# Kernel optimization log

Measured on AMD Instinct MI355X. Metric: run time of the kernel, lower is better.

Reference implementation:

```python
import jax, jax.numpy as jnp
import numpy as np

C_ATOM = 128; C_PAIR = 16; H = 4; DH = 32; BQ = 32; BK = 128
N_ATOMS = 11776; NB = N_ATOMS // BQ; N_TOK = 512
C_TOK = 384; C_TP = 128; C_TP_IN = 32; N_LAYERS = 3

def _ln(x):
    mu = jnp.mean(x, axis=-1, keepdims=True)
    xc = x - mu
    var = jnp.mean(xc * xc, axis=-1, keepdims=True)
    return xc * jax.lax.rsqrt(var + 1e-5)

def setup_inputs():
    key = jax.random.key(0)
    ks = jax.random.split(key, 32)
    rn = lambda k, s, sc=0.02: jax.random.normal(k, s, jnp.float32) * sc
    q_idx = jnp.arange(N_ATOMS, dtype=jnp.int32).reshape(NB, BQ)
    centers = jnp.arange(NB, dtype=jnp.int32) * BQ + BQ // 2
    win = centers[:, None] + jnp.arange(-BK // 2, BK // 2, dtype=jnp.int32)[None, :]
    k_mask = (win >= 0) & (win < N_ATOMS)
    k_idx = jnp.clip(win, 0, N_ATOMS - 1)
    return {
        'atom_feats': jax.random.normal(ks[0], (1, N_ATOMS, C_ATOM), jnp.float32),
        'token_pair_feats': jax.random.normal(ks[1], (1, N_TOK, N_TOK, C_TP_IN), jnp.float32),
        'W_cond': rn(ks[2], (C_ATOM, C_ATOM)),
        'W_ph': rn(ks[3], (C_PAIR, C_ATOM)),
        'W_pw': rn(ks[4], (C_PAIR, C_ATOM)),
        'W_mlp1': rn(ks[5], (C_PAIR, C_PAIR)),
        'W_mlp2': rn(ks[6], (C_PAIR, C_PAIR)),
        'pb_ln_w': jnp.ones((C_PAIR,), jnp.float32),
        'pb_ln_b': jnp.zeros((C_PAIR,), jnp.float32),
        'pb_w': rn(ks[7], (H, C_PAIR)),
        'sln_w': rn(ks[8], (N_LAYERS, 2 * C_ATOM, C_ATOM)),
        'qkv_w': rn(ks[9], (N_LAYERS, 3 * C_ATOM, C_ATOM)),
        'q_bias': rn(ks[10], (N_LAYERS, C_ATOM)),
        'out_w': rn(ks[11], (N_LAYERS, C_ATOM, C_ATOM)),
        'out_b': jnp.zeros((N_LAYERS, C_ATOM), jnp.float32),
        'ada_w': rn(ks[12], (N_LAYERS, 2 * C_ATOM, C_ATOM)),
        'ta_w': rn(ks[13], (N_LAYERS, 4 * C_ATOM, C_ATOM)),
        'tb_w': rn(ks[14], (N_LAYERS, C_ATOM, 2 * C_ATOM)),
        'gate_w': rn(ks[15], (N_LAYERS, C_ATOM, C_ATOM)),
        'gate_b': jnp.full((N_LAYERS, C_ATOM), -2.0, jnp.float32),
        'W_tok': rn(ks[16], (C_TOK, C_ATOM)),
        'W_trunk': rn(ks[17], (C_TOK, C_TOK)),
        'W_struct': rn(ks[18], (C_TOK, C_TOK)),
        'W_pairin': rn(ks[19], (C_TP, C_TP_IN)),
        'W_outer': rn(ks[20], (2 * C_TP, C_TOK)),
        'q_idx': q_idx, 'k_idx': k_idx, 'k_mask': k_mask,
        'atom_to_token': jnp.sort(jax.random.randint(ks[21], (N_ATOMS,), 0, N_TOK, dtype=jnp.int32)),
    }

def _forward(atom_feats, token_pair_feats, W_cond, W_ph, W_pw, W_mlp1, W_mlp2,
             pb_ln_w, pb_ln_b, pb_w, sln_w, qkv_w, q_bias, out_w, out_b,
             ada_w, ta_w, tb_w, gate_w, gate_b, W_tok, W_trunk, W_struct,
             W_pairin, W_outer, q_idx, k_idx, k_mask, atom_to_token):
    c = atom_feats @ W_cond.T                       # [1,N,128] atom conditioning
    s_ln = _ln(c)                                   # shared normed conditioning
    # ---- blocked pair representation + pair-to-bias ----
    cq = jax.nn.relu(s_ln[:, q_idx])                # [1,NB,BQ,128]
    ck = jax.nn.relu(s_ln[:, k_idx])                # [1,NB,BK,128]
    p = (cq @ W_ph.T)[:, :, :, None, :] + (ck @ W_pw.T)[:, :, None, :, :]  # [1,NB,BQ,BK,16]
    p = p + jax.nn.relu(jax.nn.relu(p) @ W_mlp1.T) @ W_mlp2.T
    pb = (_ln(p) * pb_ln_w + pb_ln_b) @ pb_w.T      # [1,NB,BQ,BK,H]
    pb = jnp.transpose(pb, (0, 1, 4, 2, 3))         # [1,NB,H,BQ,BK]
    neg = jnp.where(k_mask[None, :, None, None, :], 0.0, -1e9)
    a = c
    scale = 1.0 / np.sqrt(DH).astype(np.float32)
    for l in range(N_LAYERS):
        # blocked local attention with AdaLN-conditioned input
        gb = s_ln @ sln_w[l].T
        x = jax.nn.sigmoid(gb[..., :C_ATOM]) * _ln(a) + gb[..., C_ATOM:]
        qkv = x @ qkv_w[l].T
        q, k, v = jnp.split(qkv, 3, axis=-1)
        q = (q + q_bias[l]).reshape(1, N_ATOMS, H, DH)
        k = k.reshape(1, N_ATOMS, H, DH)
        v = v.reshape(1, N_ATOMS, H, DH)
        qb = q[:, q_idx]; kb = k[:, k_idx]; vb = v[:, k_idx]
        sc = jnp.einsum('bnqhd,bnkhd->bnhqk', qb, kb) * scale + pb + neg
        att = jax.nn.softmax(sc, axis=-1)
        o = jnp.einsum('bnhqk,bnkhd->bnqhd', att, vb).reshape(1, N_ATOMS, C_ATOM)
        a = a + o @ out_w[l].T + out_b[l]
        # AdaLN-modulated SwiGLU transition with adaLN-zero gate (bias init -2)
        gb2 = s_ln @ ada_w[l].T
        xt = jax.nn.sigmoid(gb2[..., :C_ATOM]) * _ln(a) + gb2[..., C_ATOM:]
        ab = xt @ ta_w[l].T
        g = jax.nn.silu(ab[..., :2 * C_ATOM]) * ab[..., 2 * C_ATOM:]
        h = g @ tb_w[l].T
        gate = jax.nn.sigmoid(s_ln @ gate_w[l].T + gate_b[l])
        a = a + gate * h
    # ---- atom -> token aggregation and output projections ----
    atom_out = jax.nn.relu(a @ W_tok.T)             # [1,N,384]
    sums = jax.ops.segment_sum(atom_out[0], atom_to_token, num_segments=N_TOK)
    cnt = jax.ops.segment_sum(jnp.ones((N_ATOMS,), atom_out.dtype), atom_to_token, num_segments=N_TOK)
    tok = (sums / jnp.maximum(cnt, 1.0)[:, None])[None]  # [1,T,384]
    s_trunk = tok @ W_trunk.T
    s_struct = tok @ W_struct.T
    u = tok @ W_outer.T                              # [1,T,256]
    pair = token_pair_feats @ W_pairin.T + u[..., :C_TP][:, :, None, :] + u[..., C_TP:][:, None, :, :]
    return s_trunk, s_struct, pair

def reference(atom_feats, token_pair_feats, W_cond, W_ph, W_pw, W_mlp1, W_mlp2,
              pb_ln_w, pb_ln_b, pb_w, sln_w, qkv_w, q_bias, out_w, out_b,
              ada_w, ta_w, tb_w, gate_w, gate_b, W_tok, W_trunk, W_struct,
              W_pairin, W_outer, q_idx, k_idx, k_mask, atom_to_token):
    return _forward(atom_feats, token_pair_feats, W_cond, W_ph, W_pw, W_mlp1, W_mlp2,
                    pb_ln_w, pb_ln_b, pb_w, sln_w, qkv_w, q_bias, out_w, out_b,
                    ada_w, ta_w, tb_w, gate_w, gate_b, W_tok, W_trunk, W_struct,
                    W_pairin, W_outer, q_idx, k_idx, k_mask, atom_to_token)
```

## Files before the change

kernel.cpp:

```cpp
#include <hip/hip_runtime.h>
#include <cstddef>

typedef unsigned short u16;
typedef __attribute__((ext_vector_type(8))) short bf8;
typedef __attribute__((ext_vector_type(4))) float f4;
typedef __attribute__((ext_vector_type(4))) unsigned short us4;

#define NATOMS 11776
#define NBLK   368

__device__ __forceinline__ u16 f2b(float x){
  union { float f; unsigned u; } v; v.f = x;
  unsigned r = v.u + 0x7fffu + ((v.u >> 16) & 1u);
  return (u16)(r >> 16);
}
__device__ __forceinline__ float b2f(u16 x){
  union { unsigned u; float f; } v; v.u = ((unsigned)x) << 16;
  return v.f;
}
__device__ __forceinline__ f4 f4zero(){ f4 z = {0.f,0.f,0.f,0.f}; return z; }
__device__ __forceinline__ f4 mfma16(bf8 a, bf8 b, f4 c){
  return __builtin_amdgcn_mfma_f32_16x16x32_bf16(a, b, c, 0, 0, 0);
}
__device__ __forceinline__ int iclamp(int v, int lo, int hi){ return v < lo ? lo : (v > hi ? hi : v); }
__device__ __forceinline__ void lds_fence(){
  asm volatile("s_waitcnt lgkmcnt(0)" ::: "memory");
  __builtin_amdgcn_sched_barrier(0);
}

struct CvtArgs {
  const float* src[13];
  u16* dst[13];
  int n4[13];
};

__global__ __launch_bounds__(256) void k_convert(CvtArgs a){
  int stride = gridDim.x * 256;
  int tid = blockIdx.x * 256 + threadIdx.x;
  for (int s = 0; s < 13; ++s){
    const float4* src = (const float4*)a.src[s];
    us4* dst = (us4*)a.dst[s];
    int n = a.n4[s];
    for (int i = tid; i < n; i += stride){
      float4 v = src[i];
      us4 o;
      o.x = f2b(v.x); o.y = f2b(v.y); o.z = f2b(v.z); o.w = f2b(v.w);
      dst[i] = o;
    }
  }
}

template<int N, int K, int LDA = K>
__device__ __forceinline__ void gemm_strip(const u16* __restrict__ A, const u16* __restrict__ W, float* L){
  constexpr int CPW = N / 4;
  constexpr int T = CPW / 16;
  const int lane = threadIdx.x & 63;
  const int wave = threadIdx.x >> 6;
  const int rr = lane & 15, grp = lane >> 4;
  f4 acc[T];
#pragma unroll
  for (int t = 0; t < T; ++t) acc[t] = f4zero();
#pragma unroll
  for (int kc = 0; kc < K / 32; ++kc){
    bf8 af = *(const bf8*)(A + rr * LDA + kc * 32 + grp * 8);
#pragma unroll
    for (int t = 0; t < T; ++t){
      const u16* wp = W + (size_t)(wave * CPW + t * 16 + rr) * K + kc * 32 + grp * 8;
      acc[t] = mfma16(af, *(const bf8*)wp, acc[t]);
    }
  }
#pragma unroll
  for (int t = 0; t < T; ++t)
#pragma unroll
    for (int r = 0; r < 4; ++r)
      L[(grp * 4 + r) * N + wave * CPW + t * 16 + rr] = acc[t][r];
}

template<int N, int K>
__global__ __launch_bounds__(256) void k_gemm_f32(const u16* __restrict__ A, const u16* __restrict__ W,
                                                  float* __restrict__ out){
  __shared__ float L[16 * N];
  const int strip = blockIdx.x;
  gemm_strip<N, K>(A + (size_t)strip * 16 * K, W, L);
  __syncthreads();
  const size_t base = (size_t)strip * 16 * N;
  for (int i = threadIdx.x; i < 16 * N; i += 256) out[base + i] = L[i];
}

__global__ __launch_bounds__(256) void k_pre(const u16* __restrict__ sln, const float* __restrict__ lnA,
                                             const u16* __restrict__ slnW, const u16* __restrict__ gateW,
                                             const u16* __restrict__ qkvW, const float* __restrict__ qb,
                                             const float* __restrict__ gbias,
                                             u16* __restrict__ qkv_out, float* __restrict__ gate_out){
  __shared__ float LB[16 * 384];
  __shared__ __align__(16) u16 X[16 * 136];
  const int strip = blockIdx.x;
  const u16* Ag = sln + (size_t)strip * 2048;
  gemm_strip<256, 128>(Ag, slnW, LB);
  __syncthreads();
  for (int i = threadIdx.x; i < 2048; i += 256){
    int r = i >> 7, c = i & 127;
    float g1 = LB[r * 256 + c], g2 = LB[r * 256 + 128 + c];
    float s = 1.f / (1.f + __expf(-g1));
    X[r * 136 + c] = f2b(s * lnA[(size_t)(strip * 16 + r) * 128 + c] + g2);
  }
  __syncthreads();
  gemm_strip<128, 128>(Ag, gateW, LB);
  __syncthreads();
  for (int i = threadIdx.x; i < 2048; i += 256){
    int c = i & 127;
    gate_out[(size_t)strip * 2048 + i] = 1.f / (1.f + __expf(-(LB[i] + gbias[c])));
  }
  __syncthreads();
  gemm_strip<384, 128, 136>(X, qkvW, LB);
  __syncthreads();
  const float scale = 0.17677669529663687f;
  for (int i = threadIdx.x; i < 16 * 384; i += 256){
    int r = i / 384, c = i - r * 384;
    float v = LB[i];
    if (c < 128) v = (v + qb[c]) * scale;
    qkv_out[(size_t)(strip * 16 + r) * 384 + c] = f2b(v);
  }
}

template<int LAST>
__global__ __launch_bounds__(256) void k_post(const u16* __restrict__ sln, float* __restrict__ lnA,
                                              float* __restrict__ a, const float* __restrict__ gate,
                                              const u16* __restrict__ adaW, const u16* __restrict__ taW,
                                              const u16* __restrict__ tbW, const u16* __restrict__ tokW,
                                              float* __restrict__ atom_out){
  __shared__ float LB[16 * 512];
  __shared__ __align__(16) u16 X[16 * 136];
  __shared__ __align__(16) u16 G[16 * 264];
  const int strip = blockIdx.x;
  const u16* Ag = sln + (size_t)strip * 2048;
  gemm_strip<256, 128>(Ag, adaW, LB);
  __syncthreads();
  for (int i = threadIdx.x; i < 2048; i += 256){
    int r = i >> 7, c = i & 127;
    float g1 = LB[r * 256 + c], g2 = LB[r * 256 + 128 + c];
    float s = 1.f / (1.f + __expf(-g1));
    X[r * 136 + c] = f2b(s * lnA[(size_t)(strip * 16 + r) * 128 + c] + g2);
  }
  __syncthreads();
  gemm_strip<512, 128, 136>(X, taW, LB);
  __syncthreads();
  for (int i = threadIdx.x; i < 16 * 256; i += 256){
    int r = i >> 8, c = i & 255;
    float ab1 = LB[r * 512 + c], ab2 = LB[r * 512 + 256 + c];
    G[r * 264 + c] = f2b(ab1 / (1.f + __expf(-ab1)) * ab2);
  }
  __syncthreads();
  gemm_strip<128, 256, 264>(G, tbW, LB);
  __syncthreads();
  for (int i = threadIdx.x; i < 2048; i += 256){
    size_t idx = (size_t)strip * 2048 + i;
    float v = a[idx] + gate[idx] * LB[i];
    a[idx] = v;
    LB[i] = v;
    if (LAST){ int r = i >> 7, c = i & 127; X[r * 136 + c] = f2b(v); }
  }
  __syncthreads();
  if (!LAST){
    int r = threadIdx.x >> 4, s = threadIdx.x & 15;
    float sum = 0.f, sq = 0.f;
#pragma unroll
    for (int j = 0; j < 8; ++j){ float v = LB[r * 128 + s * 8 + j]; sum += v; sq += v * v; }
#pragma unroll
    for (int m = 1; m < 16; m <<= 1){ sum += __shfl_xor(sum, m); sq += __shfl_xor(sq, m); }
    float mu = sum * (1.f / 128.f);
    float var = sq * (1.f / 128.f) - mu * mu;
    float rs = rsqrtf(var + 1e-5f);
#pragma unroll
    for (int j = 0; j < 8; ++j){
      int c = s * 8 + j;
      lnA[(size_t)(strip * 16 + r) * 128 + c] = (LB[r * 128 + c] - mu) * rs;
    }
  } else {
    gemm_strip<384, 128, 136>(X, tokW, LB);
    __syncthreads();
    const size_t base = (size_t)strip * 16 * 384;
    for (int i = threadIdx.x; i < 16 * 384; i += 256) atom_out[base + i] = fmaxf(LB[i], 0.f);
  }
}

__global__ __launch_bounds__(256) void k_ln_phpw(const float* __restrict__ c, float* __restrict__ lnA,
                                                 u16* __restrict__ slnb, const float* __restrict__ Wph,
                                                 const float* __restrict__ Wpw, float* __restrict__ ph,
                                                 float* __restrict__ pw){
  __shared__ float rs[4][128];
  const int wave = threadIdx.x >> 6, lane = threadIdx.x & 63;
  const int row = blockIdx.x * 4 + wave;
  const float* cr = c + (size_t)row * 128;
  float2 v = *(const float2*)(cr + lane * 2);
  float sum = v.x + v.y, sq = v.x * v.x + v.y * v.y;
#pragma unroll
  for (int m = 1; m < 64; m <<= 1){ sum += __shfl_xor(sum, m); sq += __shfl_xor(sq, m); }
  float mu = sum * (1.f / 128.f);
  float var = sq * (1.f / 128.f) - mu * mu;
  float r = rsqrtf(var + 1e-5f);
  float s0 = (v.x - mu) * r, s1 = (v.y - mu) * r;
  size_t base = (size_t)row * 128 + lane * 2;
  lnA[base] = s0; lnA[base + 1] = s1;
  slnb[base] = f2b(s0); slnb[base + 1] = f2b(s1);
  rs[wave][lane * 2] = fmaxf(s0, 0.f); rs[wave][lane * 2 + 1] = fmaxf(s1, 0.f);
  __syncthreads();
  int h = lane & 15, part = lane >> 4;
  float acch = 0.f, accw = 0.f;
#pragma unroll
  for (int k = 0; k < 32; ++k){
    int kk = part * 32 + k;
    float rv = rs[wave][kk];
    acch += rv * Wph[h * 128 + kk];
    accw += rv * Wpw[h * 128 + kk];
  }
  acch += __shfl_xor(acch, 16); acch += __shfl_xor(acch, 32);
  accw += __shfl_xor(accw, 16); accw += __shfl_xor(accw, 32);
  if (lane < 16){
    ph[(size_t)row * 16 + h] = acch;
    pw[(size_t)row * 16 + h] = accw;
  }
}

__global__ __launch_bounds__(256) void k_pb(const float* __restrict__ ph, const float* __restrict__ pw,
                                            const float* __restrict__ W1, const float* __restrict__ W2,
                                            const float* __restrict__ lnw, const float* __restrict__ lnb,
                                            const float* __restrict__ pbw, float* __restrict__ bias){
  __shared__ __align__(16) u16 mt[4][16 * 24];
  __shared__ __align__(16) u16 vt[4][16 * 24];
  const int t = threadIdx.x;
  const int lane = t & 63, wave = t >> 6;
  const int rr = lane & 15, grp = lane >> 4;
  const int b = blockIdx.x >> 3, qg = blockIdx.x & 7;
  const int q = qg * 4 + wave;
  const int qa = b * 32 + q;

  bf8 wf1 = {0,0,0,0,0,0,0,0}, wf2 = {0,0,0,0,0,0,0,0};
  bf8 bproj = {0,0,0,0,0,0,0,0}, bones = {0,0,0,0,0,0,0,0};
  if (grp < 2){
#pragma unroll
    for (int j = 0; j < 8; ++j){
      wf1[j] = (short)f2b(W1[rr * 16 + grp * 8 + j]);
      wf2[j] = (short)f2b(W2[rr * 16 + grp * 8 + j]);
      bones[j] = (short)0x3F80;
    }
    if (rr < 4){
#pragma unroll
      for (int j = 0; j < 8; ++j)
        bproj[j] = (short)f2b(pbw[rr * 16 + grp * 8 + j] * lnw[grp * 8 + j]);
    }
  }
  float w2s_r = 0.f, bb_r = 0.f;
  if (rr < 4){
#pragma unroll
    for (int cc = 0; cc < 16; ++cc){
      float pv = pbw[rr * 16 + cc];
      w2s_r += pv * lnw[cc];
      bb_r  += pv * lnb[cc];
    }
  }
  const float* phq = ph + (size_t)qa * 16;
  float pha[8];
  if (grp < 2){
#pragma unroll
    for (int j = 0; j < 8; ++j) pha[j] = phq[grp * 8 + j];
  }
  const float ph_r = phq[rr];
  u16* mw = &mt[wave][0];
  u16* vw = &vt[wave][0];

  for (int kt = 0; kt < 8; ++kt){
    const int k0 = kt * 16;
    bf8 af = {0,0,0,0,0,0,0,0};
    if (grp < 2){
      int winA = b * 32 + k0 + rr - 48;
      int kaA = iclamp(winA, 0, NATOMS - 1);
      const float* pwr = pw + (size_t)kaA * 16 + grp * 8;
#pragma unroll
      for (int j = 0; j < 8; ++j) af[j] = (short)f2b(fmaxf(pha[j] + pwr[j], 0.f));
    }
    f4 c1 = mfma16(af, wf1, f4zero());
#pragma unroll
    for (int r = 0; r < 4; ++r)
      mw[(grp * 4 + r) * 24 + rr] = f2b(fmaxf(c1[r], 0.f));
    lds_fence();
    bf8 mf = {0,0,0,0,0,0,0,0};
    if (grp < 2) mf = *(const bf8*)(mw + rr * 24 + grp * 8);
    f4 c2 = mfma16(mf, wf2, f4zero());
#pragma unroll
    for (int r = 0; r < 4; ++r){
      int win = b * 32 + k0 + grp * 4 + r - 48;
      int ka = iclamp(win, 0, NATOMS - 1);
      float v = c2[r] + ph_r + pw[(size_t)ka * 16 + rr];
      vw[(grp * 4 + r) * 24 + rr] = f2b(v);
    }
    lds_fence();
    bf8 vf = {0,0,0,0,0,0,0,0}, vf2 = {0,0,0,0,0,0,0,0};
    if (grp < 2){
      vf = *(const bf8*)(vw + rr * 24 + grp * 8);
#pragma unroll
      for (int j = 0; j < 8; ++j){
        float x = b2f((u16)vf[j]);
        union { float f; unsigned u; } s; s.f = x * x;
        vf2[j] = (short)(u16)(s.u >> 16);
      }
    }
    f4 T1 = mfma16(vf, bproj, f4zero());
    f4 T2 = mfma16(vf, bones, f4zero());
    f4 T3 = mfma16(vf2, bones, f4zero());
    if (rr < 4){
      float4 o;
      float ov[4];
#pragma unroll
      for (int r = 0; r < 4; ++r){
        int win = b * 32 + k0 + grp * 4 + r - 48;
        bool valid = (win >= 0) && (win < NATOMS);
        float S = T2[r], Q = T3[r], d = T1[r];
        float mu = S * (1.f / 16.f);
        float var = Q * (1.f / 16.f) - mu * mu;
        float rq = rsqrtf(var + 1e-5f);
        ov[r] = rq * (d - mu * w2s_r) + bb_r + (valid ? 0.f : -1e9f);
      }
      o.x = ov[0]; o.y = ov[1]; o.z = ov[2]; o.w = ov[3];
      *(float4*)(bias + ((size_t)((b * 4 + rr) * 32) + q) * 128 + k0 + grp * 4) = o;
    }
  }
}

__global__ __launch_bounds__(256) void k_attn(const u16* __restrict__ qkv, const float* __restrict__ bias,
                                              const u16* __restrict__ outw, const float* __restrict__ outb,
                                              float* __restrict__ a, float* __restrict__ lnA){
  __shared__ u16 VT[128][136];
  __shared__ u16 P[4][32 * 136];
  __shared__ u16 O[32][136];
  __shared__ float aL[32][128];
  const int t = threadIdx.x;
  const int lane = t & 63, wave = t >> 6;
  const int b = blockIdx.x;
  const int rr = lane & 15, grp = lane >> 4;

  for (int i = 0; i < 8; ++i){
    int s = t + 256 * i;
    int ka = s & 127, d0 = (s >> 7) * 8;
    int win = b * 32 + ka - 48;
    int src = iclamp(win, 0, NATOMS - 1);
    bf8 v = *(const bf8*)(qkv + (size_t)src * 384 + 256 + d0);
#pragma unroll
    for (int j = 0; j < 8; ++j) VT[d0 + j][ka] = (u16)v[j];
  }
  __syncthreads();

  const int h = wave;
  bf8 kfr[8];
#pragma unroll
  for (int kt = 0; kt < 8; ++kt){
    int ka = kt * 16 + rr;
    int win = b * 32 + ka - 48;
    int src = iclamp(win, 0, NATOMS - 1);
    kfr[kt] = *(const bf8*)(qkv + (size_t)src * 384 + 128 + h * 32 + grp * 8);
  }
  f4 S[2][8];
#pragma unroll
  for (int qt = 0; qt < 2; ++qt){
    bf8 qf = *(const bf8*)(qkv + (size_t)(b * 32 + qt * 16 + rr) * 384 + h * 32 + grp * 8);
#pragma unroll
    for (int kt = 0; kt < 8; ++kt){
      S[qt][kt] = f4zero();
      S[qt][kt] = mfma16(qf, kfr[kt], S[qt][kt]);
    }
  }
  const float* brow = bias + (size_t)((b * 4 + h) * 32) * 128;
#pragma unroll
  for (int qt = 0; qt < 2; ++qt){
#pragma unroll
    for (int r = 0; r < 4; ++r){
      int q = qt * 16 + grp * 4 + r;
      float vals[8];
      float mx = -1e30f;
#pragma unroll
      for (int kt = 0; kt < 8; ++kt){
        float v = S[qt][kt][r] + brow[q * 128 + kt * 16 + rr];
        vals[kt] = v;
        mx = fmaxf(mx, v);
      }
#pragma unroll
      for (int m = 1; m < 16; m <<= 1) mx = fmaxf(mx, __shfl_xor(mx, m));
      float sum = 0.f;
#pragma unroll
      for (int kt = 0; kt < 8; ++kt){ vals[kt] = __expf(vals[kt] - mx); sum += vals[kt]; }
#pragma unroll
      for (int m = 1; m < 16; m <<= 1) sum += __shfl_xor(sum, m);
      float inv = 1.f / sum;
#pragma unroll
      for (int kt = 0; kt < 8; ++kt)
        P[h][q * 136 + kt * 16 + rr] = f2b(vals[kt] * inv);
    }
  }
  __syncthreads();
  f4 oacc[2][2];
#pragma unroll
  for (int qt = 0; qt < 2; ++qt)
#pragma unroll
    for (int dt = 0; dt < 2; ++dt) oacc[qt][dt] = f4zero();
#pragma unroll
  for (int kc = 0; kc < 4; ++kc){
#pragma unroll
    for (int qt = 0; qt < 2; ++qt){
      bf8 pa = *(const bf8*)(&P[h][(qt * 16 + rr) * 136 + kc * 32 + grp * 8]);
#pragma unroll
      for (int dt = 0; dt < 2; ++dt){
        bf8 vb = *(const bf8*)(&VT[h * 32 + dt * 16 + rr][kc * 32 + grp * 8]);
        oacc[qt][dt] = mfma16(pa, vb, oacc[qt][dt]);
      }
    }
  }
#pragma unroll
  for (int qt = 0; qt < 2; ++qt)
#pragma unroll
    for (int dt = 0; dt < 2; ++dt)
#pragma unroll
      for (int r = 0; r < 4; ++r)
        O[qt * 16 + grp * 4 + r][h * 32 + dt * 16 + rr] = f2b(oacc[qt][dt][r]);
  __syncthreads();
  f4 pacc[2][2];
#pragma unroll
  for (int qt = 0; qt < 2; ++qt)
#pragma unroll
    for (int ct = 0; ct < 2; ++ct) pacc[qt][ct] = f4zero();
#pragma unroll
  for (int kc = 0; kc < 4; ++kc){
    bf8 a0 = *(const bf8*)(&O[rr][kc * 32 + grp * 8]);
    bf8 a1 = *(const bf8*)(&O[16 + rr][kc * 32 + grp * 8]);
#pragma unroll
    for (int ct = 0; ct < 2; ++ct){
      bf8 wf = *(const bf8*)(outw + (size_t)(wave * 32 + ct * 16 + rr) * 128 + kc * 32 + grp * 8);
      pacc[0][ct] = mfma16(a0, wf, pacc[0][ct]);
      pacc[1][ct] = mfma16(a1, wf, pacc[1][ct]);
    }
  }
#pragma unroll
  for (int qt = 0; qt < 2; ++qt)
#pragma unroll
    for (int ct = 0; ct < 2; ++ct)
#pragma unroll
      for (int r = 0; r < 4; ++r){
        int q = qt * 16 + grp * 4 + r;
        int col = wave * 32 + ct * 16 + rr;
        size_t idx = (size_t)(b * 32 + q) * 128 + col;
        float v = a[idx] + pacc[qt][ct][r] + outb[col];
        a[idx] = v;
        aL[q][col] = v;
      }
  __syncthreads();
  {
    int r = t >> 3, s8 = t & 7;
    float sum = 0.f, sq = 0.f;
#pragma unroll
    for (int j = 0; j < 16; ++j){ float v = aL[r][s8 * 16 + j]; sum += v; sq += v * v; }
#pragma unroll
    for (int m = 1; m < 8; m <<= 1){ sum += __shfl_xor(sum, m); sq += __shfl_xor(sq, m); }
    float mu = sum * (1.f / 128.f);
    float var = sq * (1.f / 128.f) - mu * mu;
    float rs = rsqrtf(var + 1e-5f);
#pragma unroll
    for (int j = 0; j < 16; ++j){
      int c = s8 * 16 + j;
      lnA[(size_t)(b * 32 + r) * 128 + c] = (aL[r][c] - mu) * rs;
    }
  }
}

__device__ __forceinline__ int lbound(const int* __restrict__ arr, int n, int v){
  int lo = 0, hi = n;
  while (lo < hi){ int mid = (lo + hi) >> 1; if (arr[mid] < v) lo = mid + 1; else hi = mid; }
  return lo;
}

__global__ __launch_bounds__(256) void k_segmean(const float* __restrict__ atom_out,
                                                 const int* __restrict__ a2t, u16* __restrict__ tokbf){
  const int tok = blockIdx.x;
  __shared__ int lo_s, hi_s;
  if (threadIdx.x == 0){
    lo_s = lbound(a2t, NATOMS, tok);
    hi_s = lbound(a2t, NATOMS, tok + 1);
  }
  __syncthreads();
  int lo = lo_s, hi = hi_s;
  float inv = 1.f / fmaxf((float)(hi - lo), 1.f);
  for (int c = threadIdx.x; c < 384; c += 256){
    float s = 0.f;
    for (int aa = lo; aa < hi; ++aa) s += atom_out[(size_t)aa * 384 + c];
    tokbf[(size_t)tok * 384 + c] = f2b(s * inv);
  }
}

__global__ __launch_bounds__(256) void k_tok(const u16* __restrict__ tok, const u16* __restrict__ catW,
                                             float* __restrict__ s_trunk, float* __restrict__ s_struct,
                                             float* __restrict__ u_f){
  __shared__ float LB[16 * 1024];
  const int strip = blockIdx.x;
  gemm_strip<1024, 384>(tok + (size_t)strip * 16 * 384, catW, LB);
  __syncthreads();
  for (int i = threadIdx.x; i < 16 * 1024; i += 256){
    int r = i >> 10, c = i & 1023;
    int row = strip * 16 + r;
    float v = LB[i];
    if (c < 384) s_trunk[(size_t)row * 384 + c] = v;
    else if (c < 768) s_struct[(size_t)row * 384 + (c - 384)] = v;
    else u_f[(size_t)row * 256 + (c - 768)] = v;
  }
}

__global__ __launch_bounds__(256) void k_pair(const float* __restrict__ tpf, const float* __restrict__ Wp,
                                              const float* __restrict__ u, float* __restrict__ out){
  const int lane = threadIdx.x & 63, wave = threadIdx.x >> 6;
  const int rr = lane & 15, grp = lane >> 4;
  const int pairbase = blockIdx.x * 64 + wave * 16;
  const int i = (blockIdx.x * 64) >> 9;
  bf8 af;
  {
    const float* tr = tpf + (size_t)(pairbase + rr) * 32 + grp * 8;
#pragma unroll
    for (int j = 0; j < 8; ++j) af[j] = (short)f2b(tr[j]);
  }
  f4 acc[8];
#pragma unroll
  for (int t = 0; t < 8; ++t){
    bf8 bf;
    const float* wr = Wp + (size_t)(t * 16 + rr) * 32 + grp * 8;
#pragma unroll
    for (int j = 0; j < 8; ++j) bf[j] = (short)f2b(wr[j]);
    acc[t] = mfma16(af, bf, f4zero());
  }
  const float* ui = u + (size_t)i * 256;
#pragma unroll
  for (int t = 0; t < 8; ++t){
    int c = t * 16 + rr;
    float uic = ui[c];
#pragma unroll
    for (int r = 0; r < 4; ++r){
      int p = pairbase + grp * 4 + r;
      int j = p & 511;
      out[(size_t)p * 128 + c] = acc[t][r] + uic + u[(size_t)j * 256 + 128 + c];
    }
  }
}

extern "C" void kernel_launch(void* const* d_in, const int* in_sizes, int n_in,
                              void* d_out, int out_size, void* d_ws, size_t ws_size,
                              hipStream_t stream){
  (void)in_sizes; (void)n_in; (void)out_size; (void)ws_size;
  const float* atom_feats = (const float*)d_in[0];
  const float* tpf        = (const float*)d_in[1];
  const float* W_cond     = (const float*)d_in[2];
  const float* W_ph       = (const float*)d_in[3];
  const float* W_pw       = (const float*)d_in[4];
  const float* W_mlp1     = (const float*)d_in[5];
  const float* W_mlp2     = (const float*)d_in[6];
  const float* pb_ln_w    = (const float*)d_in[7];
  const float* pb_ln_b    = (const float*)d_in[8];
  const float* pb_w       = (const float*)d_in[9];
  const float* sln_w      = (const float*)d_in[10];
  const float* qkv_w      = (const float*)d_in[11];
  const float* q_bias     = (const float*)d_in[12];
  const float* out_w      = (const float*)d_in[13];
  const float* out_b      = (const float*)d_in[14];
  const float* ada_w      = (const float*)d_in[15];
  const float* ta_w       = (const float*)d_in[16];
  const float* tb_w       = (const float*)d_in[17];
  const float* gate_w     = (const float*)d_in[18];
  const float* gate_b     = (const float*)d_in[19];
  const float* W_tok      = (const float*)d_in[20];
  const float* W_trunk    = (const float*)d_in[21];
  const float* W_struct   = (const float*)d_in[22];
  const float* W_pairin   = (const float*)d_in[23];
  const float* W_outer    = (const float*)d_in[24];
  const int*   a2t        = (const int*)d_in[28];

  char* wsb = (char*)d_ws;
  size_t off = 0;
  auto alc = [&](size_t bytes) -> void* {
    void* r = wsb + off;
    off = (off + bytes + 255) & ~(size_t)255;
    return r;
  };

  u16* af_bf     = (u16*)alc((size_t)NATOMS * 128 * 2);
  u16* wcond_bf  = (u16*)alc(16384 * 2);
  u16* sln_bfw   = (u16*)alc(98304 * 2);
  u16* qkv_bfw   = (u16*)alc(147456 * 2);
  u16* out_bfw   = (u16*)alc(49152 * 2);
  u16* ada_bfw   = (u16*)alc(98304 * 2);
  u16* ta_bfw    = (u16*)alc(196608 * 2);
  u16* tb_bfw    = (u16*)alc(98304 * 2);
  u16* gate_bfw  = (u16*)alc(49152 * 2);
  u16* tok_bfw   = (u16*)alc(49152 * 2);
  u16* trunk_bfw = (u16*)alc(147456 * 2);
  u16* struct_bfw= (u16*)alc(147456 * 2);
  u16* outer_bfw = (u16*)alc(98304 * 2);
  float* a_f     = (float*)alc((size_t)NATOMS * 128 * 4);
  float* lnA     = (float*)alc((size_t)NATOMS * 128 * 4);
  u16* sln_bf    = (u16*)alc((size_t)NATOMS * 128 * 2);
  u16* qkv_bf    = (u16*)alc((size_t)NATOMS * 384 * 2);
  float* gate_f  = (float*)alc((size_t)NATOMS * 128 * 4);
  float* ph      = (float*)alc((size_t)NATOMS * 16 * 4);
  float* pw      = (float*)alc((size_t)NATOMS * 16 * 4);
  float* bias    = (float*)alc((size_t)NBLK * 4 * 32 * 128 * 4);
  float* atom_out= bias;
  u16* tok_bf    = (u16*)alc(512 * 384 * 2);
  float* u_f     = (float*)alc(512 * 256 * 4);

  float* s_trunk  = (float*)d_out;
  float* s_struct = s_trunk + 512 * 384;
  float* pair_out = s_struct + 512 * 384;

  CvtArgs ca;
  const float* srcs[13] = {atom_feats, W_cond, sln_w, qkv_w, out_w, ada_w, ta_w, tb_w,
                           gate_w, W_tok, W_trunk, W_struct, W_outer};
  u16* dsts[13] = {af_bf, wcond_bf, sln_bfw, qkv_bfw, out_bfw, ada_bfw, ta_bfw, tb_bfw,
                   gate_bfw, tok_bfw, trunk_bfw, struct_bfw, outer_bfw};
  int n4s[13] = {NATOMS * 128 / 4, 4096, 24576, 36864, 12288, 24576, 49152, 24576,
                 12288, 12288, 36864, 36864, 24576};
  for (int s = 0; s < 13; ++s){ ca.src[s] = srcs[s]; ca.dst[s] = dsts[s]; ca.n4[s] = n4s[s]; }
  k_convert<<<512, 256, 0, stream>>>(ca);

  k_gemm_f32<128, 128><<<736, 256, 0, stream>>>(af_bf, wcond_bf, a_f);
  k_ln_phpw<<<2944, 256, 0, stream>>>(a_f, lnA, sln_bf, W_ph, W_pw, ph, pw);
  k_pb<<<NBLK * 8, 256, 0, stream>>>(ph, pw, W_mlp1, W_mlp2, pb_ln_w, pb_ln_b, pb_w, bias);

  for (int l = 0; l < 3; ++l){
    const u16* slnW  = sln_bfw  + (size_t)l * 256 * 128;
    const u16* qkvW  = qkv_bfw  + (size_t)l * 384 * 128;
    const u16* outW  = out_bfw  + (size_t)l * 128 * 128;
    const u16* adaW  = ada_bfw  + (size_t)l * 256 * 128;
    const u16* taW   = ta_bfw   + (size_t)l * 512 * 128;
    const u16* tbW   = tb_bfw   + (size_t)l * 128 * 256;
    const u16* gateW = gate_bfw + (size_t)l * 128 * 128;
    k_pre<<<736, 256, 0, stream>>>(sln_bf, lnA, slnW, gateW, qkvW,
                                   q_bias + l * 128, gate_b + l * 128, qkv_bf, gate_f);
    k_attn<<<NBLK, 256, 0, stream>>>(qkv_bf, bias, outW, out_b + l * 128, a_f, lnA);
    if (l < 2)
      k_post<0><<<736, 256, 0, stream>>>(sln_bf, lnA, a_f, gate_f, adaW, taW, tbW,
                                         tok_bfw, atom_out);
    else
      k_post<1><<<736, 256, 0, stream>>>(sln_bf, lnA, a_f, gate_f, adaW, taW, tbW,
                                         tok_bfw, atom_out);
  }

  k_segmean<<<512, 256, 0, stream>>>(atom_out, a2t, tok_bf);
  k_tok<<<32, 256, 0, stream>>>(tok_bf, trunk_bfw, s_trunk, s_struct, u_f);
  k_pair<<<4096, 256, 0, stream>>>(tpf, W_pairin, u_f, pair_out);
}
```

Before: 433.9 us.

## Fuse cond GEMM with layernorm/pair projections, move gate into post, register LN in attn

Replaces the bf16 conversion of atom_feats, the separate W_cond GEMM and the LN/ph/pw kernel with one k_cond kernel that converts fp32 to bf16 on the fly and does LN plus the ph/pw projections via MFMA. The gate GEMM moves from k_pre into k_post and its values stay in registers, so the fp32 gate buffer is never written or read back. The attention epilogue computes the layernorm from registers with shuffles and a small partial-sum array instead of staging a 32x128 fp32 tile in LDS. This cuts launches and global traffic, at the cost of more register pressure in k_post and ph/pw now computed in bf16 instead of fp32.

```diff
diff --git a/kernel.cpp b/kernel.cpp
--- a/kernel.cpp
+++ b/kernel.cpp
@@ -27,17 +27,24 @@
   asm volatile("s_waitcnt lgkmcnt(0)" ::: "memory");
   __builtin_amdgcn_sched_barrier(0);
 }
+__device__ __forceinline__ bf8 cvt_f32x8(const float* __restrict__ p){
+  float4 a = *(const float4*)p, b = *(const float4*)(p + 4);
+  bf8 o;
+  o[0] = (short)f2b(a.x); o[1] = (short)f2b(a.y); o[2] = (short)f2b(a.z); o[3] = (short)f2b(a.w);
+  o[4] = (short)f2b(b.x); o[5] = (short)f2b(b.y); o[6] = (short)f2b(b.z); o[7] = (short)f2b(b.w);
+  return o;
+}
 
 struct CvtArgs {
-  const float* src[13];
-  u16* dst[13];
-  int n4[13];
+  const float* src[11];
+  u16* dst[11];
+  int n4[11];
 };
 
 __global__ __launch_bounds__(256) void k_convert(CvtArgs a){
   int stride = gridDim.x * 256;
   int tid = blockIdx.x * 256 + threadIdx.x;
-  for (int s = 0; s < 13; ++s){
+  for (int s = 0; s < 11; ++s){
     const float4* src = (const float4*)a.src[s];
     us4* dst = (us4*)a.dst[s];
     int n = a.n4[s];
@@ -76,22 +83,77 @@
       L[(grp * 4 + r) * N + wave * CPW + t * 16 + rr] = acc[t][r];
 }
 
-template<int N, int K>
-__global__ __launch_bounds__(256) void k_gemm_f32(const u16* __restrict__ A, const u16* __restrict__ W,
-                                                  float* __restrict__ out){
-  __shared__ float L[16 * N];
+__global__ __launch_bounds__(256) void k_cond(const float* __restrict__ af, const float* __restrict__ Wc,
+                                              const float* __restrict__ Wph, const float* __restrict__ Wpw,
+                                              float* __restrict__ a_f, float* __restrict__ lnA,
+                                              u16* __restrict__ sln_bf, float* __restrict__ ph,
+                                              float* __restrict__ pw){
+  __shared__ float LB[16 * 128];
+  __shared__ __align__(16) u16 X[16 * 136];
   const int strip = blockIdx.x;
-  gemm_strip<N, K>(A + (size_t)strip * 16 * K, W, L);
-  __syncthreads();
-  const size_t base = (size_t)strip * 16 * N;
-  for (int i = threadIdx.x; i < 16 * N; i += 256) out[base + i] = L[i];
+  const int lane = threadIdx.x & 63, wave = threadIdx.x >> 6;
+  const int rr = lane & 15, grp = lane >> 4;
+  {
+    f4 acc[2];
+    acc[0] = f4zero(); acc[1] = f4zero();
+#pragma unroll
+    for (int kc = 0; kc < 4; ++kc){
+      bf8 afr = cvt_f32x8(af + (size_t)(strip * 16 + rr) * 128 + kc * 32 + grp * 8);
+#pragma unroll
+      for (int t = 0; t < 2; ++t){
+        bf8 bfr = cvt_f32x8(Wc + (size_t)(wave * 32 + t * 16 + rr) * 128 + kc * 32 + grp * 8);
+        acc[t] = mfma16(afr, bfr, acc[t]);
+      }
+    }
+#pragma unroll
+    for (int t = 0; t < 2; ++t)
+#pragma unroll
+      for (int r = 0; r < 4; ++r)
+        LB[(grp * 4 + r) * 128 + wave * 32 + t * 16 + rr] = acc[t][r];
+  }
+  __syncthreads();
+  {
+    int r = threadIdx.x >> 4, s = threadIdx.x & 15;
+    float sum = 0.f, sq = 0.f;
+#pragma unroll
+    for (int j = 0; j < 8; ++j){ float v = LB[r * 128 + s * 8 + j]; sum += v; sq += v * v; }
+#pragma unroll
+    for (int m = 1; m < 16; m <<= 1){ sum += __shfl_xor(sum, m); sq += __shfl_xor(sq, m); }
+    float mu = sum * (1.f / 128.f);
+    float var = sq * (1.f / 128.f) - mu * mu;
+    float rs = rsqrtf(var + 1e-5f);
+#pragma unroll
+    for (int j = 0; j < 8; ++j){
+      int c = s * 8 + j;
+      float v = LB[r * 128 + c];
+      size_t idx = (size_t)(strip * 16 + r) * 128 + c;
+      a_f[idx] = v;
+      float ln = (v - mu) * rs;
+      lnA[idx] = ln;
+      sln_bf[idx] = f2b(ln);
+      X[r * 136 + c] = f2b(fmaxf(ln, 0.f));
+    }
+  }
+  __syncthreads();
+  if (wave < 2){
+    const float* Wsel = wave ? Wpw : Wph;
+    f4 acc = f4zero();
+#pragma unroll
+    for (int kc = 0; kc < 4; ++kc){
+      bf8 afr = *(const bf8*)(&X[rr * 136 + kc * 32 + grp * 8]);
+      bf8 bfr = cvt_f32x8(Wsel + (size_t)rr * 128 + kc * 32 + grp * 8);
+      acc = mfma16(afr, bfr, acc);
+    }
+    float* out = wave ? pw : ph;
+#pragma unroll
+    for (int r = 0; r < 4; ++r)
+      out[(size_t)(strip * 16 + grp * 4 + r) * 16 + rr] = acc[r];
+  }
 }
 
 __global__ __launch_bounds__(256) void k_pre(const u16* __restrict__ sln, const float* __restrict__ lnA,
-                                             const u16* __restrict__ slnW, const u16* __restrict__ gateW,
-                                             const u16* __restrict__ qkvW, const float* __restrict__ qb,
-                                             const float* __restrict__ gbias,
-                                             u16* __restrict__ qkv_out, float* __restrict__ gate_out){
+                                             const u16* __restrict__ slnW, const u16* __restrict__ qkvW,
+                                             const float* __restrict__ qb, u16* __restrict__ qkv_out){
   __shared__ float LB[16 * 384];
   __shared__ __align__(16) u16 X[16 * 136];
   const int strip = blockIdx.x;
@@ -103,13 +165,6 @@
     float g1 = LB[r * 256 + c], g2 = LB[r * 256 + 128 + c];
     float s = 1.f / (1.f + __expf(-g1));
     X[r * 136 + c] = f2b(s * lnA[(size_t)(strip * 16 + r) * 128 + c] + g2);
-  }
-  __syncthreads();
-  gemm_strip<128, 128>(Ag, gateW, LB);
-  __syncthreads();
-  for (int i = threadIdx.x; i < 2048; i += 256){
-    int c = i & 127;
-    gate_out[(size_t)strip * 2048 + i] = 1.f / (1.f + __expf(-(LB[i] + gbias[c])));
   }
   __syncthreads();
   gemm_strip<384, 128, 136>(X, qkvW, LB);
@@ -125,7 +180,8 @@
 
 template<int LAST>
 __global__ __launch_bounds__(256) void k_post(const u16* __restrict__ sln, float* __restrict__ lnA,
-                                              float* __restrict__ a, const float* __restrict__ gate,
+                                              float* __restrict__ a,
+                                              const u16* __restrict__ gateW, const float* __restrict__ gbias,
                                               const u16* __restrict__ adaW, const u16* __restrict__ taW,
                                               const u16* __restrict__ tbW, const u16* __restrict__ tokW,
                                               float* __restrict__ atom_out){
@@ -134,6 +190,16 @@
   __shared__ __align__(16) u16 G[16 * 264];
   const int strip = blockIdx.x;
   const u16* Ag = sln + (size_t)strip * 2048;
+  float gv[8];
+  gemm_strip<128, 128>(Ag, gateW, LB);
+  __syncthreads();
+#pragma unroll
+  for (int ii = 0; ii < 8; ++ii){
+    int i = threadIdx.x + 256 * ii;
+    int c = i & 127;
+    gv[ii] = 1.f / (1.f + __expf(-(LB[i] + gbias[c])));
+  }
+  __syncthreads();
   gemm_strip<256, 128>(Ag, adaW, LB);
   __syncthreads();
   for (int i = threadIdx.x; i < 2048; i += 256){
@@ -153,9 +219,11 @@
   __syncthreads();
   gemm_strip<128, 256, 264>(G, tbW, LB);
   __syncthreads();
-  for (int i = threadIdx.x; i < 2048; i += 256){
+#pragma unroll
+  for (int ii = 0; ii < 8; ++ii){
+    int i = threadIdx.x + 256 * ii;
     size_t idx = (size_t)strip * 2048 + i;
-    float v = a[idx] + gate[idx] * LB[i];
+    float v = a[idx] + gv[ii] * LB[i];
     a[idx] = v;
     LB[i] = v;
     if (LAST){ int r = i >> 7, c = i & 127; X[r * 136 + c] = f2b(v); }
@@ -181,44 +249,6 @@
     __syncthreads();
     const size_t base = (size_t)strip * 16 * 384;
     for (int i = threadIdx.x; i < 16 * 384; i += 256) atom_out[base + i] = fmaxf(LB[i], 0.f);
-  }
-}
-
-__global__ __launch_bounds__(256) void k_ln_phpw(const float* __restrict__ c, float* __restrict__ lnA,
-                                                 u16* __restrict__ slnb, const float* __restrict__ Wph,
-                                                 const float* __restrict__ Wpw, float* __restrict__ ph,
-                                                 float* __restrict__ pw){
-  __shared__ float rs[4][128];
-  const int wave = threadIdx.x >> 6, lane = threadIdx.x & 63;
-  const int row = blockIdx.x * 4 + wave;
-  const float* cr = c + (size_t)row * 128;
-  float2 v = *(const float2*)(cr + lane * 2);
-  float sum = v.x + v.y, sq = v.x * v.x + v.y * v.y;
-#pragma unroll
-  for (int m = 1; m < 64; m <<= 1){ sum += __shfl_xor(sum, m); sq += __shfl_xor(sq, m); }
-  float mu = sum * (1.f / 128.f);
-  float var = sq * (1.f / 128.f) - mu * mu;
-  float r = rsqrtf(var + 1e-5f);
-  float s0 = (v.x - mu) * r, s1 = (v.y - mu) * r;
-  size_t base = (size_t)row * 128 + lane * 2;
-  lnA[base] = s0; lnA[base + 1] = s1;
-  slnb[base] = f2b(s0); slnb[base + 1] = f2b(s1);
-  rs[wave][lane * 2] = fmaxf(s0, 0.f); rs[wave][lane * 2 + 1] = fmaxf(s1, 0.f);
-  __syncthreads();
-  int h = lane & 15, part = lane >> 4;
-  float acch = 0.f, accw = 0.f;
-#pragma unroll
-  for (int k = 0; k < 32; ++k){
-    int kk = part * 32 + k;
-    float rv = rs[wave][kk];
-    acch += rv * Wph[h * 128 + kk];
-    accw += rv * Wpw[h * 128 + kk];
-  }
-  acch += __shfl_xor(acch, 16); acch += __shfl_xor(acch, 32);
-  accw += __shfl_xor(accw, 16); accw += __shfl_xor(accw, 32);
-  if (lane < 16){
-    ph[(size_t)row * 16 + h] = acch;
-    pw[(size_t)row * 16 + h] = accw;
   }
 }
 
@@ -333,7 +363,7 @@
   __shared__ u16 VT[128][136];
   __shared__ u16 P[4][32 * 136];
   __shared__ u16 O[32][136];
-  __shared__ float aL[32][128];
+  __shared__ float part2[32][8];
   const int t = threadIdx.x;
   const int lane = t & 63, wave = t >> 6;
   const int b = blockIdx.x;
@@ -438,6 +468,7 @@
       pacc[1][ct] = mfma16(a1, wf, pacc[1][ct]);
     }
   }
+  float vv[2][2][4];
 #pragma unroll
   for (int qt = 0; qt < 2; ++qt)
 #pragma unroll
@@ -449,25 +480,41 @@
         size_t idx = (size_t)(b * 32 + q) * 128 + col;
         float v = a[idx] + pacc[qt][ct][r] + outb[col];
         a[idx] = v;
-        aL[q][col] = v;
-      }
-  __syncthreads();
-  {
-    int r = t >> 3, s8 = t & 7;
-    float sum = 0.f, sq = 0.f;
-#pragma unroll
-    for (int j = 0; j < 16; ++j){ float v = aL[r][s8 * 16 + j]; sum += v; sq += v * v; }
-#pragma unroll
-    for (int m = 1; m < 8; m <<= 1){ sum += __shfl_xor(sum, m); sq += __shfl_xor(sq, m); }
-    float mu = sum * (1.f / 128.f);
-    float var = sq * (1.f / 128.f) - mu * mu;
-    float rs = rsqrtf(var + 1e-5f);
-#pragma unroll
-    for (int j = 0; j < 16; ++j){
-      int c = s8 * 16 + j;
-      lnA[(size_t)(b * 32 + r) * 128 + c] = (aL[r][c] - mu) * rs;
-    }
-  }
+        vv[qt][ct][r] = v;
+      }
+#pragma unroll
+  for (int qt = 0; qt < 2; ++qt)
+#pragma unroll
+    for (int r = 0; r < 4; ++r){
+      float ps = vv[qt][0][r] + vv[qt][1][r];
+      float pq = vv[qt][0][r] * vv[qt][0][r] + vv[qt][1][r] * vv[qt][1][r];
+#pragma unroll
+      for (int m = 1; m < 16; m <<= 1){ ps += __shfl_xor(ps, m); pq += __shfl_xor(pq, m); }
+      if (rr == 0){
+        int q = qt * 16 + grp * 4 + r;
+        part2[q][wave * 2] = ps;
+        part2[q][wave * 2 + 1] = pq;
+      }
+    }
+  __syncthreads();
+#pragma unroll
+  for (int qt = 0; qt < 2; ++qt)
+#pragma unroll
+    for (int r = 0; r < 4; ++r){
+      int q = qt * 16 + grp * 4 + r;
+      f4 p0 = *(const f4*)&part2[q][0];
+      f4 p1 = *(const f4*)&part2[q][4];
+      float S = p0[0] + p0[2] + p1[0] + p1[2];
+      float Q = p0[1] + p0[3] + p1[1] + p1[3];
+      float mu = S * (1.f / 128.f);
+      float var = Q * (1.f / 128.f) - mu * mu;
+      float rs = rsqrtf(var + 1e-5f);
+#pragma unroll
+      for (int ct = 0; ct < 2; ++ct){
+        int col = wave * 32 + ct * 16 + rr;
+        lnA[(size_t)(b * 32 + q) * 128 + col] = (vv[qt][ct][r] - mu) * rs;
+      }
+    }
 }
 
 __device__ __forceinline__ int lbound(const int* __restrict__ arr, int n, int v){
@@ -585,8 +632,6 @@
     return r;
   };
 
-  u16* af_bf     = (u16*)alc((size_t)NATOMS * 128 * 2);
-  u16* wcond_bf  = (u16*)alc(16384 * 2);
   u16* sln_bfw   = (u16*)alc(98304 * 2);
   u16* qkv_bfw   = (u16*)alc(147456 * 2);
   u16* out_bfw   = (u16*)alc(49152 * 2);
@@ -602,7 +647,6 @@
   float* lnA     = (float*)alc((size_t)NATOMS * 128 * 4);
   u16* sln_bf    = (u16*)alc((size_t)NATOMS * 128 * 2);
   u16* qkv_bf    = (u16*)alc((size_t)NATOMS * 384 * 2);
-  float* gate_f  = (float*)alc((size_t)NATOMS * 128 * 4);
   float* ph      = (float*)alc((size_t)NATOMS * 16 * 4);
   float* pw      = (float*)alc((size_t)NATOMS * 16 * 4);
   float* bias    = (float*)alc((size_t)NBLK * 4 * 32 * 128 * 4);
@@ -615,17 +659,16 @@
   float* pair_out = s_struct + 512 * 384;
 
   CvtArgs ca;
-  const float* srcs[13] = {atom_feats, W_cond, sln_w, qkv_w, out_w, ada_w, ta_w, tb_w,
-                           gate_w, W_tok, W_trunk, W_struct, W_outer};
-  u16* dsts[13] = {af_bf, wcond_bf, sln_bfw, qkv_bfw, out_bfw, ada_bfw, ta_bfw, tb_bfw,
-                   gate_bfw, tok_bfw, trunk_bfw, struct_bfw, outer_bfw};
-  int n4s[13] = {NATOMS * 128 / 4, 4096, 24576, 36864, 12288, 24576, 49152, 24576,
-                 12288, 12288, 36864, 36864, 24576};
-  for (int s = 0; s < 13; ++s){ ca.src[s] = srcs[s]; ca.dst[s] = dsts[s]; ca.n4[s] = n4s[s]; }
-  k_convert<<<512, 256, 0, stream>>>(ca);
-
-  k_gemm_f32<128, 128><<<736, 256, 0, stream>>>(af_bf, wcond_bf, a_f);
-  k_ln_phpw<<<2944, 256, 0, stream>>>(a_f, lnA, sln_bf, W_ph, W_pw, ph, pw);
+  const float* srcs[11] = {sln_w, qkv_w, out_w, ada_w, ta_w, tb_w, gate_w,
+                           W_tok, W_trunk, W_struct, W_outer};
+  u16* dsts[11] = {sln_bfw, qkv_bfw, out_bfw, ada_bfw, ta_bfw, tb_bfw, gate_bfw,
+                   tok_bfw, trunk_bfw, struct_bfw, outer_bfw};
+  int n4s[11] = {24576, 36864, 12288, 24576, 49152, 24576, 12288,
+                 12288, 36864, 36864, 24576};
+  for (int s = 0; s < 11; ++s){ ca.src[s] = srcs[s]; ca.dst[s] = dsts[s]; ca.n4[s] = n4s[s]; }
+  k_convert<<<256, 256, 0, stream>>>(ca);
+
+  k_cond<<<736, 256, 0, stream>>>(atom_feats, W_cond, W_ph, W_pw, a_f, lnA, sln_bf, ph, pw);
   k_pb<<<NBLK * 8, 256, 0, stream>>>(ph, pw, W_mlp1, W_mlp2, pb_ln_w, pb_ln_b, pb_w, bias);
 
   for (int l = 0; l < 3; ++l){
@@ -636,15 +679,14 @@
     const u16* taW   = ta_bfw   + (size_t)l * 512 * 128;
     const u16* tbW   = tb_bfw   + (size_t)l * 128 * 256;
     const u16* gateW = gate_bfw + (size_t)l * 128 * 128;
-    k_pre<<<736, 256, 0, stream>>>(sln_bf, lnA, slnW, gateW, qkvW,
-                                   q_bias + l * 128, gate_b + l * 128, qkv_bf, gate_f);
+    k_pre<<<736, 256, 0, stream>>>(sln_bf, lnA, slnW, qkvW, q_bias + l * 128, qkv_bf);
     k_attn<<<NBLK, 256, 0, stream>>>(qkv_bf, bias, outW, out_b + l * 128, a_f, lnA);
     if (l < 2)
-      k_post<0><<<736, 256, 0, stream>>>(sln_bf, lnA, a_f, gate_f, adaW, taW, tbW,
-                                         tok_bfw, atom_out);
+      k_post<0><<<736, 256, 0, stream>>>(sln_bf, lnA, a_f, gateW, gate_b + l * 128,
+                                         adaW, taW, tbW, tok_bfw, atom_out);
     else
-      k_post<1><<<736, 256, 0, stream>>>(sln_bf, lnA, a_f, gate_f, adaW, taW, tbW,
-                                         tok_bfw, atom_out);
+      k_post<1><<<736, 256, 0, stream>>>(sln_bf, lnA, a_f, gateW, gate_b + l * 128,
+                                         adaW, taW, tbW, tok_bfw, atom_out);
   }
 
   k_segmean<<<512, 256, 0, stream>>>(atom_out, a2t, tok_bf);
```

Measured after the change: 390.6 us. -10.0%, faster.
